# Kernel optimization log

Measured on AMD Instinct MI355X. Metric: run time of the kernel, lower is better.

Reference implementation:

```python
import jax, jax.numpy as jnp
import numpy as np

QLEN, MLEN, BSZ, DM, NH, DH, DI = 512, 512, 8, 1024, 16, 64, 4096
KLEN = QLEN + MLEN
EPS = 1e-5
NEG = -1e30


def layer_norm(x, g, b):
    mu = jnp.mean(x, axis=-1, keepdims=True)
    var = jnp.mean(jnp.square(x - mu), axis=-1, keepdims=True)
    return (x - mu) * jax.lax.rsqrt(var + EPS) * g + b


def rel_shift(x):
    # x: [qlen, rlen, bsz, n_head] -> Transformer-XL relative shift
    q, r, b, n = x.shape
    zp = jnp.zeros((q, 1, b, n), x.dtype)
    xp = jnp.concatenate([zp, x], axis=1).reshape(r + 1, q, b, n)
    return xp[1:].reshape(q, r, b, n)


def setup_inputs() -> dict:
    key = jax.random.key(0)
    ks = jax.random.split(key, 12)
    inp = {
        "w": jax.random.normal(ks[0], (QLEN, BSZ, DM), jnp.float32),
        "r": jax.random.normal(ks[1], (KLEN, DM), jnp.float32),
        "mems": jax.random.normal(ks[2], (MLEN, BSZ, DM), jnp.float32),
        "w_qkv": jax.random.normal(ks[3], (DM, 3 * NH * DH), jnp.float32) * 0.02,
        "w_r": jax.random.normal(ks[4], (DM, NH * DH), jnp.float32) * 0.02,
        "w_o": jax.random.normal(ks[5], (NH * DH, DM), jnp.float32) * 0.02,
        "r_w_bias": jax.random.normal(ks[6], (NH, DH), jnp.float32) * 0.02,
        "r_r_bias": jax.random.normal(ks[7], (NH, DH), jnp.float32) * 0.02,
        "ln1_g": jnp.ones((DM,), jnp.float32),
        "ln1_b": jnp.zeros((DM,), jnp.float32),
        "ff_w1": jax.random.normal(ks[8], (DM, DI), jnp.float32) * 0.02,
        "ff_b1": jnp.zeros((DI,), jnp.float32),
        "ff_w2": jax.random.normal(ks[9], (DI, DM), jnp.float32) * 0.02,
        "ff_b2": jnp.zeros((DM,), jnp.float32),
        "ln2_g": jnp.ones((DM,), jnp.float32),
        "ln2_b": jnp.zeros((DM,), jnp.float32),
    }
    # causal mask with memory: query i (global pos MLEN+i) cannot attend to j > MLEN+i
    i = jnp.arange(QLEN)[:, None]
    j = jnp.arange(KLEN)[None, :]
    inp["attn_mask"] = j > (i + MLEN)
    return inp


def reference(w, r, mems, attn_mask, w_qkv, w_r, w_o, r_w_bias, r_r_bias,
              ln1_g, ln1_b, ff_w1, ff_b1, ff_w2, ff_b2, ln2_g, ln2_b):
    qlen, bsz = w.shape[0], w.shape[1]
    scale = 1.0 / (DH ** 0.5)
    cat = jnp.concatenate([mems, w], axis=0)                 # [klen, b, d]
    klen = cat.shape[0]
    heads = cat @ w_qkv                                      # [klen, b, 3*H*D]
    hq, hk, hv = jnp.split(heads, 3, axis=-1)
    hq = hq[-qlen:].reshape(qlen, bsz, NH, DH)
    hk = hk.reshape(klen, bsz, NH, DH)
    hv = hv.reshape(klen, bsz, NH, DH)
    r_head_k = (r @ w_r).reshape(klen, NH, DH)               # [rlen, H, D]

    AC = jnp.einsum('ibnd,jbnd->ijbn', hq + r_w_bias, hk)
    BD = rel_shift(jnp.einsum('ibnd,jnd->ijbn', hq + r_r_bias, r_head_k))
    score = (AC + BD) * scale                                # [q, k, b, h]
    score = jnp.where(attn_mask[:, :, None, None], NEG, score)
    prob = jax.nn.softmax(score, axis=1)
    vec = jnp.einsum('ijbn,jbnd->ibnd', prob, hv).reshape(qlen, bsz, NH * DH)
    attn_out = vec @ w_o
    h = layer_norm(w + attn_out, ln1_g, ln1_b)               # post-LN
    ff = jax.nn.relu(h @ ff_w1 + ff_b1) @ ff_w2 + ff_b2
    return layer_norm(h + ff, ln2_g, ln2_b)
```

## Files before the change

### kernel.cpp

```cpp
#include <hip/hip_runtime.h>
#include <hip/hip_bf16.h>

#define QLEN 512
#define MLEN 512
#define KLEN 1024
#define BSZ 8
#define DM 1024
#define NH 16
#define DH 64
#define DI 4096
#define NEGF (-1e30f)

typedef unsigned short u16;
typedef __attribute__((ext_vector_type(8))) short short8;
typedef __attribute__((ext_vector_type(4))) short s16x4;
typedef __attribute__((ext_vector_type(4))) float f32x4;

__device__ __forceinline__ float bf2f(u16 u) {
    union { unsigned i; float f; } x; x.i = ((unsigned)u) << 16; return x.f;
}
__device__ __forceinline__ u16 f2bf(float f) {
    __hip_bfloat16 h = __float2bfloat16(f);
    return *reinterpret_cast<u16*>(&h);
}
__device__ __forceinline__ float4 ldg4(const float* p) {
    return *reinterpret_cast<const float4*>(p);
}
__device__ __forceinline__ void gload16(const void* g, void* l) {
    __builtin_amdgcn_global_load_lds(
        (const __attribute__((address_space(1))) void*)g,
        (__attribute__((address_space(3))) void*)l, 16, 0, 0);
}

__global__ __launch_bounds__(256) void cast2_kernel(
    const float* __restrict__ a, const float* __restrict__ b, int splitE,
    u16* __restrict__ out, int n)
{
    int idx = (blockIdx.x * 256 + threadIdx.x) * 4;
    if (idx >= n) return;
    const float* src = (idx < splitE) ? (a + idx) : (b + (idx - splitE));
    float4 v = ldg4(src);
    u16 o[4] = { f2bf(v.x), f2bf(v.y), f2bf(v.z), f2bf(v.w) };
    *reinterpret_cast<uint2*>(&out[idx]) = *reinterpret_cast<uint2*>(o);
}

__device__ __forceinline__ void tr32(
    const float* __restrict__ W, u16* __restrict__ WT, int K, int N, int k0, int n0)
{
    __shared__ float tile[32][33];
    const int tx = threadIdx.x & 31, ty = threadIdx.x >> 5;
    #pragma unroll
    for (int j = 0; j < 4; ++j)
        tile[ty + j * 8][tx] = W[(size_t)(k0 + ty + j * 8) * N + n0 + tx];
    __syncthreads();
    #pragma unroll
    for (int j = 0; j < 4; ++j)
        WT[(size_t)(n0 + ty + j * 8) * K + k0 + tx] = f2bf(tile[tx][ty + j * 8]);
}

__global__ __launch_bounds__(256) void transpose_all(
    const float* __restrict__ w_qkv, u16* __restrict__ qkvT,
    const float* __restrict__ w_r,   u16* __restrict__ wrT,
    const float* __restrict__ w_o,   u16* __restrict__ woT,
    const float* __restrict__ ffw1,  u16* __restrict__ f1T,
    const float* __restrict__ ffw2,  u16* __restrict__ f2T)
{
    int id = blockIdx.x;
    if (id < 3072)       { int l = id;        tr32(w_qkv, qkvT, 1024, 3072, (l / 96) * 32, (l % 96) * 32); }
    else if (id < 4096)  { int l = id - 3072; tr32(w_r,   wrT,  1024, 1024, (l / 32) * 32, (l % 32) * 32); }
    else if (id < 5120)  { int l = id - 4096; tr32(w_o,   woT,  1024, 1024, (l / 32) * 32, (l % 32) * 32); }
    else if (id < 9216)  { int l = id - 5120; tr32(ffw1,  f1T,  1024, 4096, (l / 128) * 32, (l % 128) * 32); }
    else                 { int l = id - 9216; tr32(ffw2,  f2T,  4096, 1024, (l / 32) * 32, (l % 32) * 32); }
}

__global__ __launch_bounds__(256) void v_transpose(
    const u16* __restrict__ heads, u16* __restrict__ Vg)
{
    const int bn = blockIdx.x;
    const int b = bn >> 4, n = bn & 15;
    const int kt = blockIdx.y;
    const int t = threadIdx.x;
    __shared__ u16 L[64 * 64];

    #pragma unroll
    for (int rep = 0; rep < 2; ++rep) {
        int idx = t + rep * 256;
        int key = idx >> 3, dc = (idx & 7) * 8;
        short8 v = *reinterpret_cast<const short8*>(
            &heads[((size_t)((kt * 64 + key) * BSZ + b)) * 3072 + 2048 + n * 64 + dc]);
        *reinterpret_cast<short8*>((char*)L + key * 128 + ((dc * 2) ^ ((key & 7) << 4))) = v;
    }
    __syncthreads();
    #pragma unroll
    for (int rep = 0; rep < 2; ++rep) {
        int idx = t + rep * 256;
        int d = idx >> 3, kc = (idx & 7) * 8;
        short8 o;
        #pragma unroll
        for (int e = 0; e < 8; ++e)
            o[e] = *(const short*)((char*)L + (kc + e) * 128 + ((d * 2) ^ (((kc + e) & 7) << 4)));
        *reinterpret_cast<short8*>(&Vg[((size_t)(bn * 64 + d)) * KLEN + kt * 64 + kc]) = o;
    }
}

template<bool BIAS, bool RELU, bool OUTBF>
__global__ __launch_bounds__(256) void gemm_mfma(
    const u16* __restrict__ A, const u16* __restrict__ BT,
    const float* __restrict__ bias,
    float* __restrict__ Cf, u16* __restrict__ Cb,
    int M, int N, int K, int lda, int ldb)
{
    __shared__ u16 As[128 * 64];
    __shared__ u16 Bs[128 * 64];
    const int bm = blockIdx.y * 128, bn = blockIdx.x * 128;
    const int z = blockIdx.z;
    A  += (size_t)z * K;
    BT += (size_t)z * K;
    const size_t zoff = (size_t)z * M * N;
    const int t = threadIdx.x;
    const int w = t >> 6, l = t & 63, lg = l >> 4, lq = l & 15;
    const int wm = (w >> 1) * 64, wn = (w & 1) * 64;
    const int r8 = l >> 3, slot = l & 7;
    const int gcol = (slot * 16) ^ (r8 << 4);

    f32x4 acc[4][4];
    #pragma unroll
    for (int x = 0; x < 4; ++x)
        #pragma unroll
        for (int y = 0; y < 4; ++y)
            acc[x][y] = (f32x4){0.f, 0.f, 0.f, 0.f};

    const int swzr = (lq & 7) << 4;

    for (int k0 = 0; k0 < K; k0 += 64) {
        __syncthreads();
        #pragma unroll
        for (int it = 0; it < 4; ++it) {
            const int base_row = w * 8 + it * 32;
            gload16((const char*)A + (((size_t)(bm + base_row + r8) * lda + k0) << 1) + gcol,
                    (char*)As + base_row * 128);
            gload16((const char*)BT + (((size_t)(bn + base_row + r8) * ldb + k0) << 1) + gcol,
                    (char*)Bs + base_row * 128);
        }
        __syncthreads();
        #pragma unroll
        for (int ks = 0; ks < 2; ++ks) {
            const int cb = (ks * 64 + 16 * lg) ^ swzr;
            short8 af[4], bf_[4];
            #pragma unroll
            for (int x = 0; x < 4; ++x)
                af[x] = *reinterpret_cast<const short8*>((char*)As + (wm + 16 * x + lq) * 128 + cb);
            #pragma unroll
            for (int y = 0; y < 4; ++y)
                bf_[y] = *reinterpret_cast<const short8*>((char*)Bs + (wn + 16 * y + lq) * 128 + cb);
            #pragma unroll
            for (int x = 0; x < 4; ++x)
                #pragma unroll
                for (int y = 0; y < 4; ++y)
                    acc[x][y] = __builtin_amdgcn_mfma_f32_16x16x32_bf16(af[x], bf_[y], acc[x][y], 0, 0, 0);
        }
    }
    #pragma unroll
    for (int x = 0; x < 4; ++x) {
        #pragma unroll
        for (int y = 0; y < 4; ++y) {
            const int col = bn + wn + 16 * y + lq;
            #pragma unroll
            for (int r = 0; r < 4; ++r) {
                const int row = bm + wm + 16 * x + 4 * lg + r;
                float v = acc[x][y][r];
                if constexpr (BIAS) { if (z == 0) v += bias[col]; }
                if constexpr (RELU) v = fmaxf(v, 0.f);
                if constexpr (OUTBF) Cb[zoff + (size_t)row * N + col] = f2bf(v);
                else                 Cf[zoff + (size_t)row * N + col] = v;
            }
        }
    }
}

template<bool BIAS, bool RELU, bool OUTBF>
__global__ __launch_bounds__(512, 2) void gemm_deep(
    const u16* __restrict__ A, const u16* __restrict__ BT,
    const float* __restrict__ bias,
    float* __restrict__ Cf, u16* __restrict__ Cb,
    int M, int N, int K, int lda, int ldb)
{
    __shared__ u16 lds[3 * 24576];
    const int bm = blockIdx.y * 256, bn = blockIdx.x * 128;
    const int z = blockIdx.z;
    A  += (size_t)z * K;
    BT += (size_t)z * K;
    const size_t zoff = (size_t)z * M * N;
    const int t = threadIdx.x;
    const int w = t >> 6, l = t & 63, lg = l >> 4, lq = l & 15;
    const int wm = (w >> 1) * 64;
    const int wn = (w & 1) * 64;
    const int srow = t >> 3, slot = t & 7;
    const int gcol = (slot * 16) ^ ((srow & 7) << 4);
    const int swzr = (lq & 7) << 4;

    auto stage_tile = [&](int kt, int buf) {
        const int k0 = kt * 64;
        char* Ab = (char*)lds + buf * 49152 + w * 1024;
        char* Bb = (char*)lds + buf * 49152 + 32768 + w * 1024;
        #pragma unroll
        for (int i = 0; i < 4; ++i)
            gload16((const char*)A + (((size_t)(bm + i * 64 + srow) * lda + k0) << 1) + gcol,
                    Ab + i * 8192);
        #pragma unroll
        for (int i = 0; i < 2; ++i)
            gload16((const char*)BT + (((size_t)(bn + i * 64 + srow) * ldb + k0) << 1) + gcol,
                    Bb + i * 8192);
    };

    f32x4 acc[4][4];
    #pragma unroll
    for (int x = 0; x < 4; ++x)
        #pragma unroll
        for (int y = 0; y < 4; ++y)
            acc[x][y] = (f32x4){0.f, 0.f, 0.f, 0.f};

    const int NT = K >> 6;
    stage_tile(0, 0);
    stage_tile(1, 1);

    for (int kt = 0; kt < NT; ++kt) {
        if (kt < NT - 1) asm volatile("s_waitcnt vmcnt(6)" ::: "memory");
        else             asm volatile("s_waitcnt vmcnt(0)" ::: "memory");
        __builtin_amdgcn_s_barrier();
        __builtin_amdgcn_sched_barrier(0);
        if (kt + 2 < NT) stage_tile(kt + 2, (kt + 2) % 3);

        const char* Ab = (const char*)lds + (kt % 3) * 49152;
        const char* Bb = Ab + 32768;
        #pragma unroll
        for (int ks = 0; ks < 2; ++ks) {
            const int cb = (ks * 64 + 16 * lg) ^ swzr;
            short8 af[4], bf_[4];
            #pragma unroll
            for (int x = 0; x < 4; ++x)
                af[x] = *reinterpret_cast<const short8*>(Ab + (wm + 16 * x + lq) * 128 + cb);
            #pragma unroll
            for (int y = 0; y < 4; ++y)
                bf_[y] = *reinterpret_cast<const short8*>(Bb + (wn + 16 * y + lq) * 128 + cb);
            __builtin_amdgcn_s_setprio(1);
            #pragma unroll
            for (int x = 0; x < 4; ++x)
                #pragma unroll
                for (int y = 0; y < 4; ++y)
                    acc[x][y] = __builtin_amdgcn_mfma_f32_16x16x32_bf16(af[x], bf_[y], acc[x][y], 0, 0, 0);
            __builtin_amdgcn_s_setprio(0);
        }
    }

    #pragma unroll
    for (int x = 0; x < 4; ++x) {
        #pragma unroll
        for (int y = 0; y < 4; ++y) {
            const int col = bn + wn + 16 * y + lq;
            #pragma unroll
            for (int r = 0; r < 4; ++r) {
                const int row = bm + wm + 16 * x + 4 * lg + r;
                float v = acc[x][y][r];
                if constexpr (BIAS) { if (z == 0) v += bias[col]; }
                if constexpr (RELU) v = fmaxf(v, 0.f);
                if constexpr (OUTBF) Cb[zoff + (size_t)row * N + col] = f2bf(v);
                else                 Cf[zoff + (size_t)row * N + col] = v;
            }
        }
    }
}

__global__ __launch_bounds__(512, 4) void attn_mfma(
    const u16* __restrict__ heads,
    const u16* __restrict__ Vg,
    const u16* __restrict__ rhk,
    const float* __restrict__ rwb, const float* __restrict__ rrb,
    u16* __restrict__ vec)
{
    const int b = blockIdx.x >> 4;
    const int n = blockIdx.x & 15;
    const int i0 = (3 - blockIdx.y) * 128;
    const int t = threadIdx.x;
    const int w = t >> 6;
    const int l = t & 63;
    const int lg = l >> 4, lq = l & 15;
    const int r8 = l >> 3, sl = l & 7;

    __shared__ u16 Ks[64 * 64];
    __shared__ u16 Vt[64 * 64];
    __shared__ u16 Rs[192 * 64];
    __shared__ u16 SbO[8 * 16 * 84];
    __shared__ u16 Ps[8 * 16 * 64];

    u16* SbW = SbO + w * 16 * 84;
    u16* PsW = Ps + w * 16 * 64;
    const int swzr = (lq & 7) << 4;
    const int stg_swz = (sl * 16) ^ (r8 << 4);

    short8 qw[2], qr[2];
    {
        const int qrow = i0 + 16 * w + lq;
        const size_t gbase = ((size_t)((MLEN + qrow) * BSZ + b)) * 3072 + n * 64;
        #pragma unroll
        for (int ks = 0; ks < 2; ++ks) {
            short8 qv = *reinterpret_cast<const short8*>(&heads[gbase + ks * 32 + 8 * lg]);
            short8 xw, xr;
            #pragma unroll
            for (int e = 0; e < 8; ++e) {
                float f = bf2f((u16)qv[e]);
                int d = ks * 32 + 8 * lg + e;
                xw[e] = (short)f2bf(f + rwb[n * 64 + d]);
                xr[e] = (short)f2bf(f + rrb[n * 64 + d]);
            }
            qw[ks] = xw; qr[ks] = xr;
        }
    }

    float m_run = NEGF, l_run = 0.f;
    f32x4 acc[4];
    #pragma unroll
    for (int df = 0; df < 4; ++df) acc[df] = (f32x4){0.f, 0.f, 0.f, 0.f};

    const int s0 = 112 - 16 * w;
    const int ntiles = i0 / 64 + 10;

    for (int tile = 0; tile < ntiles; ++tile) {
        const int j0 = tile << 6;
        __syncthreads();
        gload16((const char*)heads
                    + (((size_t)((j0 + w * 8 + r8) * BSZ + b)) * 3072 + 1024 + n * 64) * 2
                    + stg_swz,
                (char*)Ks + w * 1024);
        gload16((const char*)Vg
                    + (((size_t)(blockIdx.x * 64 + w * 8 + r8)) * KLEN + j0) * 2
                    + stg_swz,
                (char*)Vt + w * 1024);
        const int obase = j0 - i0 + 384;
        #pragma unroll
        for (int pass = 0; pass < 3; ++pass) {
            int row = pass * 64 + w * 8 + r8;
            int o = obase + row;
            o = o > (KLEN - 1) ? (KLEN - 1) : o;
            gload16((const char*)rhk + ((size_t)o * 1024 + n * 64) * 2 + stg_swz,
                    (char*)Rs + pass * 8192 + w * 1024);
        }
        __syncthreads();

        __builtin_amdgcn_s_setprio(1);
        #pragma unroll
        for (int ff = 0; ff < 5; ++ff) {
            f32x4 d = (f32x4){0.f, 0.f, 0.f, 0.f};
            #pragma unroll
            for (int ks = 0; ks < 2; ++ks) {
                short8 a = *reinterpret_cast<const short8*>(
                    (char*)Rs + (s0 + 16 * ff + lq) * 128 + ((ks * 64 + 16 * lg) ^ swzr));
                d = __builtin_amdgcn_mfma_f32_16x16x32_bf16(a, qr[ks], d, 0, 0, 0);
            }
            s16x4 pk;
            #pragma unroll
            for (int r = 0; r < 4; ++r) pk[r] = (short)f2bf(d[r]);
            *reinterpret_cast<s16x4*>(&SbW[lq * 84 + 16 * ff + 4 * lg]) = pk;
        }
        f32x4 dac[4];
        #pragma unroll
        for (int f = 0; f < 4; ++f) {
            f32x4 d = (f32x4){0.f, 0.f, 0.f, 0.f};
            #pragma unroll
            for (int ks = 0; ks < 2; ++ks) {
                short8 a = *reinterpret_cast<const short8*>(
                    (char*)Ks + (16 * f + lq) * 128 + ((ks * 64 + 16 * lg) ^ swzr));
                d = __builtin_amdgcn_mfma_f32_16x16x32_bf16(a, qw[ks], d, 0, 0, 0);
            }
            dac[f] = d;
        }
        __builtin_amdgcn_s_setprio(0);

        const bool fullTile = (i0 + 16 * w + MLEN - j0) >= 63;
        float sv[4][4];
        float mx = NEGF;
        if (fullTile) {
            #pragma unroll
            for (int f = 0; f < 4; ++f)
                #pragma unroll
                for (int r = 0; r < 4; ++r) {
                    int k = 16 * f + 4 * lg + r;
                    float bd = bf2f(SbW[lq * 84 + k - lq + 15]);
                    float x = (dac[f][r] + bd) * 0.125f;
                    sv[f][r] = x;
                    mx = fmaxf(mx, x);
                }
        } else {
            const int bound = i0 + 16 * w + lq + MLEN - j0;
            #pragma unroll
            for (int f = 0; f < 4; ++f)
                #pragma unroll
                for (int r = 0; r < 4; ++r) {
                    int k = 16 * f + 4 * lg + r;
                    float bd = bf2f(SbW[lq * 84 + k - lq + 15]);
                    float x = (k <= bound) ? (dac[f][r] + bd) * 0.125f : NEGF;
                    sv[f][r] = x;
                    mx = fmaxf(mx, x);
                }
        }
        mx = fmaxf(mx, __shfl_xor(mx, 16));
        mx = fmaxf(mx, __shfl_xor(mx, 32));
        float m_new = fmaxf(m_run, mx);
        float alpha = __expf(m_run - m_new);
        float ps = 0.f;
        #pragma unroll
        for (int f = 0; f < 4; ++f) {
            s16x4 pk;
            #pragma unroll
            for (int r = 0; r < 4; ++r) {
                float p = __expf(sv[f][r] - m_new);
                ps += p;
                pk[r] = (short)f2bf(p);
            }
            *reinterpret_cast<s16x4*>(
                (char*)PsW + lq * 128 + (((4 * f + lg) ^ ((lq & 7) << 1)) << 3)) = pk;
        }
        ps += __shfl_xor(ps, 16);
        ps += __shfl_xor(ps, 32);
        l_run = l_run * alpha + ps;
        m_run = m_new;

        float alr[4];
        #pragma unroll
        for (int r = 0; r < 4; ++r) alr[r] = __shfl(alpha, 20 * lg + r);
        __builtin_amdgcn_s_setprio(1);
        #pragma unroll
        for (int df = 0; df < 4; ++df) {
            f32x4 a = acc[df];
            #pragma unroll
            for (int r = 0; r < 4; ++r) a[r] *= alr[r];
            #pragma unroll
            for (int ks = 0; ks < 2; ++ks) {
                short8 pa = *reinterpret_cast<const short8*>(
                    (char*)PsW + lq * 128 + ((ks * 64 + 16 * lg) ^ swzr));
                short8 vb = *reinterpret_cast<const short8*>(
                    (char*)Vt + (16 * df + lq) * 128 + ((ks * 64 + 16 * lg) ^ swzr));
                a = __builtin_amdgcn_mfma_f32_16x16x32_bf16(pa, vb, a, 0, 0, 0);
            }
            acc[df] = a;
        }
        __builtin_amdgcn_s_setprio(0);
    }

    float inv[4];
    #pragma unroll
    for (int r = 0; r < 4; ++r) inv[r] = 1.f / __shfl(l_run, 20 * lg + r);
    #pragma unroll
    for (int df = 0; df < 4; ++df) {
        #pragma unroll
        for (int r = 0; r < 4; ++r) {
            const int il = 16 * w + 4 * lg + r;
            float o = acc[df][r] * inv[r];
            vec[((size_t)((i0 + il) * BSZ + b)) * DM + n * 64 + 16 * df + lq] = f2bf(o);
        }
    }
}

template<int NRES, bool WB>
__global__ __launch_bounds__(256) void ln_res_kernel(
    const float* __restrict__ x, const float* __restrict__ res,
    const float* __restrict__ res2,
    const float* __restrict__ g, const float* __restrict__ bta,
    float* __restrict__ out, u16* __restrict__ outb)
{
    const int row = blockIdx.x;
    const int t = threadIdx.x;
    const int lane = t & 63, wv = t >> 6;
    __shared__ float red0[4], red1[4];

    float4 a = ldg4(&x[(size_t)row * DM + t * 4]);
    float4 b = ldg4(&res[(size_t)row * DM + t * 4]);
    float v0 = a.x + b.x, v1 = a.y + b.y, v2 = a.z + b.z, v3 = a.w + b.w;
    if constexpr (NRES == 2) {
        float4 c = ldg4(&res2[(size_t)row * DM + t * 4]);
        v0 += c.x; v1 += c.y; v2 += c.z; v3 += c.w;
    }
    float s = v0 + v1 + v2 + v3;
    #pragma unroll
    for (int o = 32; o; o >>= 1) s += __shfl_xor(s, o);
    if (lane == 0) red0[wv] = s;
    __syncthreads();
    float mu = (red0[0] + red0[1] + red0[2] + red0[3]) * (1.f / DM);
    float d0 = v0 - mu, d1 = v1 - mu, d2 = v2 - mu, d3 = v3 - mu;
    float q = d0*d0 + d1*d1 + d2*d2 + d3*d3;
    #pragma unroll
    for (int o = 32; o; o >>= 1) q += __shfl_xor(q, o);
    if (lane == 0) red1[wv] = q;
    __syncthreads();
    float var = (red1[0] + red1[1] + red1[2] + red1[3]) * (1.f / DM);
    float rs = rsqrtf(var + 1e-5f);
    float4 gv = ldg4(&g[t * 4]);
    float4 bv = ldg4(&bta[t * 4]);
    float o0 = d0 * rs * gv.x + bv.x;
    float o1 = d1 * rs * gv.y + bv.y;
    float o2 = d2 * rs * gv.z + bv.z;
    float o3 = d3 * rs * gv.w + bv.w;
    float4 o4 = make_float4(o0, o1, o2, o3);
    *reinterpret_cast<float4*>(&out[(size_t)row * DM + t * 4]) = o4;
    if constexpr (WB) {
        u16 ob[4] = { f2bf(o0), f2bf(o1), f2bf(o2), f2bf(o3) };
        *reinterpret_cast<uint2*>(&outb[(size_t)row * DM + t * 4]) = *reinterpret_cast<uint2*>(ob);
    }
}

extern "C" void kernel_launch(void* const* d_in, const int* in_sizes, int n_in,
                              void* d_out, int out_size, void* d_ws, size_t ws_size,
                              hipStream_t stream) {
    const float* w     = (const float*)d_in[0];
    const float* r     = (const float*)d_in[1];
    const float* mems  = (const float*)d_in[2];
    const float* w_qkv = (const float*)d_in[3];
    const float* w_r   = (const float*)d_in[4];
    const float* w_o   = (const float*)d_in[5];
    const float* rwb   = (const float*)d_in[6];
    const float* rrb   = (const float*)d_in[7];
    const float* ln1g  = (const float*)d_in[8];
    const float* ln1b  = (const float*)d_in[9];
    const float* ffw1  = (const float*)d_in[10];
    const float* ffb1  = (const float*)d_in[11];
    const float* ffw2  = (const float*)d_in[12];
    const float* ffb2  = (const float*)d_in[13];
    const float* ln2g  = (const float*)d_in[14];
    const float* ln2b  = (const float*)d_in[15];
    (void)in_sizes; (void)n_in; (void)out_size; (void)ws_size;

    char* p = (char*)d_ws;
    auto alloc = [&](size_t bytes) { char* q = p; p += (bytes + 255) & ~(size_t)255; return q; };
    u16* catB   = (u16*)alloc((size_t)8192 * 1024 * 2);
    u16* rB     = (u16*)alloc((size_t)1024 * 1024 * 2);
    u16* qkvT   = (u16*)alloc((size_t)3072 * 1024 * 2);
    u16* wrT    = (u16*)alloc((size_t)1024 * 1024 * 2);
    u16* woT    = (u16*)alloc((size_t)1024 * 1024 * 2);
    u16* f1T    = (u16*)alloc((size_t)4096 * 1024 * 2);
    u16* f2T    = (u16*)alloc((size_t)1024 * 4096 * 2);
    u16* heads  = (u16*)alloc((size_t)8192 * 3072 * 2);
    u16* rhk    = (u16*)alloc((size_t)1024 * 1024 * 2);
    u16* vec    = (u16*)alloc((size_t)4096 * 1024 * 2);
    u16* hB     = (u16*)alloc((size_t)4096 * 1024 * 2);
    u16* ff1    = (u16*)alloc((size_t)4096 * 4096 * 2);
    float* hF   = (float*)alloc((size_t)4096 * 1024 * 4);

    u16* Vg = catB;
    float* attn_out = (float*)ff1;
    float* ff2 = (float*)heads;
    float* outp = (float*)d_out;

    cast2_kernel<<<8192, 256, 0, stream>>>(mems, w, 4096 * 1024, catB, 8192 * 1024);
    cast2_kernel<<<1024, 256, 0, stream>>>(r, r, 1024 * 1024, rB, 1024 * 1024);
    transpose_all<<<13312, 256, 0, stream>>>(w_qkv, qkvT, w_r, wrT, w_o, woT,
                                             ffw1, f1T, ffw2, f2T);

    gemm_deep<false, false, true><<<dim3(24, 32), 512, 0, stream>>>(
        catB, qkvT, nullptr, nullptr, heads, 8192, 3072, 1024, 1024, 1024);
    v_transpose<<<dim3(128, 16), 256, 0, stream>>>(heads, Vg);
    gemm_mfma<false, false, true><<<dim3(8, 8), 256, 0, stream>>>(
        rB, wrT, nullptr, nullptr, rhk, 1024, 1024, 1024, 1024, 1024);
    attn_mfma<<<dim3(BSZ * NH, QLEN / 128), 512, 0, stream>>>(
        heads, Vg, rhk, rwb, rrb, vec);
    gemm_mfma<false, false, false><<<dim3(8, 32, 2), 256, 0, stream>>>(
        vec, woT, nullptr, attn_out, nullptr, 4096, 1024, 512, 1024, 1024);
    ln_res_kernel<2, true><<<4096, 256, 0, stream>>>(
        w, attn_out, attn_out + (size_t)4096 * 1024, ln1g, ln1b, hF, hB);
    gemm_deep<true, true, true><<<dim3(32, 16), 512, 0, stream>>>(
        hB, f1T, ffb1, nullptr, ff1, 4096, 4096, 1024, 1024, 1024);
    gemm_deep<true, false, false><<<dim3(8, 16, 2), 512, 0, stream>>>(
        ff1, f2T, ffb2, ff2, nullptr, 4096, 1024, 2048, 4096, 4096);
    ln_res_kernel<2, false><<<4096, 256, 0, stream>>>(
        hF, ff2, ff2 + (size_t)4096 * 1024, ln2g, ln2b, outp, nullptr);
}
```

Baseline: 328.4 us.

## Split GEMM prefetch across k-substeps, skip masked attention tiles, defer softmax rescale

The GEMM prefetch of the next-but-one tile is now issued in two halves, one inside each k-substep after the fragment loads, with an extra barrier after the first. This interleaves global loads with MFMA work. The attention loop skips a warp's whole tile when it is fully causally masked. The online softmax only rescales the accumulator when the new max exceeds the running max by more than a threshold, which saves exp and multiplies but lets unnormalized values grow. The masked-tile skip runs after a __syncthreads and uses continue, so warps may diverge across later barriers, and vmcnt(6) may no longer match the split load pattern.

```diff
diff --git a/kernel.cpp b/kernel.cpp
--- a/kernel.cpp
+++ b/kernel.cpp
@@ -199,18 +199,16 @@
     const int gcol = (slot * 16) ^ ((srow & 7) << 4);
     const int swzr = (lq & 7) << 4;
 
-    auto stage_tile = [&](int kt, int buf) {
+    auto stage_half = [&](int kt, int buf, int half) {
         const int k0 = kt * 64;
         char* Ab = (char*)lds + buf * 49152 + w * 1024;
         char* Bb = (char*)lds + buf * 49152 + 32768 + w * 1024;
         #pragma unroll
-        for (int i = 0; i < 4; ++i)
-            gload16((const char*)A + (((size_t)(bm + i * 64 + srow) * lda + k0) << 1) + gcol,
-                    Ab + i * 8192);
-        #pragma unroll
         for (int i = 0; i < 2; ++i)
-            gload16((const char*)BT + (((size_t)(bn + i * 64 + srow) * ldb + k0) << 1) + gcol,
-                    Bb + i * 8192);
+            gload16((const char*)A + (((size_t)(bm + (half * 2 + i) * 64 + srow) * lda + k0) << 1) + gcol,
+                    Ab + (half * 2 + i) * 8192);
+        gload16((const char*)BT + (((size_t)(bn + half * 64 + srow) * ldb + k0) << 1) + gcol,
+                Bb + half * 8192);
     };
 
     f32x4 acc[4][4];
@@ -221,18 +219,20 @@
             acc[x][y] = (f32x4){0.f, 0.f, 0.f, 0.f};
 
     const int NT = K >> 6;
-    stage_tile(0, 0);
-    stage_tile(1, 1);
+    stage_half(0, 0, 0); stage_half(0, 0, 1);
+    stage_half(1, 1, 0); stage_half(1, 1, 1);
 
     for (int kt = 0; kt < NT; ++kt) {
         if (kt < NT - 1) asm volatile("s_waitcnt vmcnt(6)" ::: "memory");
         else             asm volatile("s_waitcnt vmcnt(0)" ::: "memory");
         __builtin_amdgcn_s_barrier();
         __builtin_amdgcn_sched_barrier(0);
-        if (kt + 2 < NT) stage_tile(kt + 2, (kt + 2) % 3);
 
         const char* Ab = (const char*)lds + (kt % 3) * 49152;
         const char* Bb = Ab + 32768;
+        const bool pf = (kt + 2 < NT);
+        const int pbuf = (kt + 2) % 3;
+
         #pragma unroll
         for (int ks = 0; ks < 2; ++ks) {
             const int cb = (ks * 64 + 16 * lg) ^ swzr;
@@ -243,6 +243,8 @@
             #pragma unroll
             for (int y = 0; y < 4; ++y)
                 bf_[y] = *reinterpret_cast<const short8*>(Bb + (wn + 16 * y + lq) * 128 + cb);
+            if (pf) stage_half(kt + 2, pbuf, ks);
+            if (ks == 0) __builtin_amdgcn_s_barrier();
             __builtin_amdgcn_s_setprio(1);
             #pragma unroll
             for (int x = 0; x < 4; ++x)
@@ -347,6 +349,9 @@
         }
         __syncthreads();
 
+        const int bmax = i0 + 16 * w + 15 + MLEN - j0;
+        if (bmax < 0) continue;
+
         __builtin_amdgcn_s_setprio(1);
         #pragma unroll
         for (int ff = 0; ff < 5; ++ff) {
@@ -405,8 +410,8 @@
         }
         mx = fmaxf(mx, __shfl_xor(mx, 16));
         mx = fmaxf(mx, __shfl_xor(mx, 32));
-        float m_new = fmaxf(m_run, mx);
-        float alpha = __expf(m_run - m_new);
+        const bool defer = (__all(mx <= m_run + 8.0f) != 0);
+        const float m_new = defer ? m_run : fmaxf(m_run, mx);
         float ps = 0.f;
         #pragma unroll
         for (int f = 0; f < 4; ++f) {
@@ -422,18 +427,25 @@
         }
         ps += __shfl_xor(ps, 16);
         ps += __shfl_xor(ps, 32);
-        l_run = l_run * alpha + ps;
-        m_run = m_new;
-
-        float alr[4];
-        #pragma unroll
-        for (int r = 0; r < 4; ++r) alr[r] = __shfl(alpha, 20 * lg + r);
+        if (defer) {
+            l_run += ps;
+        } else {
+            float alpha = __expf(m_run - m_new);
+            l_run = l_run * alpha + ps;
+            m_run = m_new;
+            float alr[4];
+            #pragma unroll
+            for (int r = 0; r < 4; ++r) alr[r] = __shfl(alpha, 20 * lg + r);
+            #pragma unroll
+            for (int df = 0; df < 4; ++df)
+                #pragma unroll
+                for (int r = 0; r < 4; ++r) acc[df][r] *= alr[r];
+        }
+
         __builtin_amdgcn_s_setprio(1);
         #pragma unroll
         for (int df = 0; df < 4; ++df) {
             f32x4 a = acc[df];
-            #pragma unroll
-            for (int r = 0; r < 4; ++r) a[r] *= alr[r];
             #pragma unroll
             for (int ks = 0; ks < 2; ++ks) {
                 short8 pa = *reinterpret_cast<const short8*>(
```

Measured after the change: 327.6 us. Within noise of the previous version (-0.2%).
